# Kernel optimization log

Hardware: AMD Instinct MI355X
Metric: run time of the kernel (lower is better)

Reference implementation:

```python
import jax, jax.numpy as jnp
import numpy as np

BATCH = 10
HID = 128
OUT = 7
MAX_LEN = 2048


def setup_inputs() -> dict:
    key = jax.random.key(0)
    ks = jax.random.split(key, 10)
    h0 = jax.random.normal(ks[0], (1, BATCH, HID), dtype=jnp.float32)
    c0 = jax.random.normal(ks[1], (1, BATCH, HID), dtype=jnp.float32)
    # target is a sequence of one-hot vectors, shape (MAX_LEN+1, 1, OUT)
    tgt_idx = jax.random.randint(ks[2], (MAX_LEN + 1,), 0, OUT)
    target_onehot = jax.nn.one_hot(tgt_idx, OUT, dtype=jnp.float32)[:, None, :]
    # per-step teacher-forcing coin flips (torch.rand(1) < 0.5 externalized)
    tf_mask = jax.random.bernoulli(ks[3], 0.5, (MAX_LEN,))
    # LSTM parameters, torch gate order [i, f, g, o]; k = 1/sqrt(HID) init scale
    k = 1.0 / np.sqrt(HID)
    W_ih = jax.random.uniform(ks[4], (4 * HID, OUT), minval=-k, maxval=k, dtype=jnp.float32)
    W_hh = jax.random.uniform(ks[5], (4 * HID, HID), minval=-k, maxval=k, dtype=jnp.float32)
    b_ih = jax.random.uniform(ks[6], (4 * HID,), minval=-k, maxval=k, dtype=jnp.float32)
    b_hh = jax.random.uniform(ks[7], (4 * HID,), minval=-k, maxval=k, dtype=jnp.float32)
    W_out = jax.random.uniform(ks[8], (OUT, HID), minval=-k, maxval=k, dtype=jnp.float32)
    b_out = jax.random.uniform(ks[9], (OUT,), minval=-k, maxval=k, dtype=jnp.float32)
    return dict(h0=h0, c0=c0, target_onehot=target_onehot, tf_mask=tf_mask,
                W_ih=W_ih, W_hh=W_hh, b_ih=b_ih, b_hh=b_hh, W_out=W_out, b_out=b_out)


def reference(h0, c0, target_onehot, tf_mask, W_ih, W_hh, b_ih, b_hh, W_out, b_out):
    # initial decoder input: one-hot at last class for all 10 batch items
    x0 = jnp.zeros((BATCH, OUT), jnp.float32).at[:, OUT - 1].set(1.0)
    tgt_next = target_onehot[1:MAX_LEN + 1, 0, :]  # (MAX_LEN, OUT), fed at step i
    bias = b_ih + b_hh

    def step(carry, inp):
        h, c, x = carry            # h,c: (B,HID); x: (B,OUT)
        tf, tgt = inp              # tf: scalar bool; tgt: (OUT,)
        xr = jax.nn.relu(x)
        gates = xr @ W_ih.T + h @ W_hh.T + bias          # (B, 4*HID)
        i_g, f_g, g_g, o_g = jnp.split(gates, 4, axis=-1)
        c2 = jax.nn.sigmoid(f_g) * c + jax.nn.sigmoid(i_g) * jnp.tanh(g_g)
        h2 = jax.nn.sigmoid(o_g) * jnp.tanh(c2)
        logits = h2 @ W_out.T + b_out                    # (B, OUT)
        greedy = jax.nn.one_hot(jnp.argmax(logits, axis=-1), OUT, dtype=jnp.float32)
        nxt = jnp.where(tf, jnp.broadcast_to(tgt, (BATCH, OUT)), greedy)
        return (h2, c2, nxt), logits

    (hT, cT, _), logits = jax.lax.scan(
        step, (h0[0], c0[0], x0), (tf_mask, tgt_next))
    logits = jnp.transpose(logits, (1, 0, 2))            # (B, MAX_LEN, OUT)
    log_probs = jax.nn.log_softmax(logits, axis=-1)
    return log_probs, (hT[None], cT[None])
```

## Files before the change

kernel.cpp:

```cpp
#include <hip/hip_runtime.h>
#include <math.h>

#define BATCH 10
#define HID 128
#define OUT 7
#define MAXLEN 2048
#define NG 512
#define NT 512
#define RINGD 512
#define OFF_STATE ((size_t)BATCH * MAXLEN * OUT)

typedef float float2v __attribute__((ext_vector_type(2)));
typedef float float4v __attribute__((ext_vector_type(4)));

__device__ __forceinline__ float sigm_(float x) { return 1.0f / (1.0f + __expf(-x)); }
__device__ __forceinline__ float tanh_(float x) { return 1.0f - 2.0f / (1.0f + __expf(2.0f * x)); }

__device__ __forceinline__ float grp8_sum(float v) {
    v += __int_as_float(__builtin_amdgcn_update_dpp(0, __float_as_int(v), 0xB1, 0xF, 0xF, true));
    v += __int_as_float(__builtin_amdgcn_update_dpp(0, __float_as_int(v), 0x4E, 0xF, 0xF, true));
    v += __int_as_float(__builtin_amdgcn_update_dpp(0, __float_as_int(v), 0x141, 0xF, 0xF, true));
    return v;
}

__global__
__attribute__((amdgpu_flat_work_group_size(NT, NT), amdgpu_waves_per_eu(2, 2)))
void decoder_rnn_kernel(const float* __restrict__ h0,
                        const float* __restrict__ c0,
                        const float* __restrict__ tonehot,
                        const void*  __restrict__ tf_raw,
                        const float* __restrict__ Wih,
                        const float* __restrict__ Whh,
                        const float* __restrict__ bih,
                        const float* __restrict__ bhh,
                        const float* __restrict__ Wout,
                        const float* __restrict__ bout,
                        float* __restrict__ out)
{
    __shared__ __align__(16) float h_lds[HID];
    __shared__ __align__(16) float gates_lds[NG];
    __shared__ float wih_eff[OUT * NG];
    __shared__ float ring[RINGD][OUT];
    __shared__ unsigned char tgt8[MAXLEN];
    __shared__ unsigned char tf8[MAXLEN];
    __shared__ int tf_byte_mode;

    const int t    = threadIdx.x;
    const int lane = t & 63;
    const int wv   = t >> 6;
    const int ksl  = lane & 7;
    const int grp  = lane >> 3;
    const int b    = blockIdx.x;
    const int gbase = wv * 64 + grp * 8;

    float2v wgt2[8][8];
    #pragma unroll
    for (int g = 0; g < 8; g++)
        #pragma unroll
        for (int p = 0; p < 8; p++) {
            const int kk = (p >> 1) * 32 + ksl * 4 + (p & 1) * 2;
            wgt2[g][p] = *(const float2v*)&Whh[(size_t)(gbase + g) * HID + kk];
        }

    float2v lw2[8];
    #pragma unroll
    for (int p = 0; p < 8; p++) { float2v z = {0.f, 0.f}; lw2[p] = z; }
    if (wv < 2 && grp < OUT) {
        #pragma unroll
        for (int p = 0; p < 8; p++) {
            const int kk = (p >> 1) * 32 + ksl * 4 + (p & 1) * 2;
            lw2[p] = *(const float2v*)&Wout[(size_t)grp * HID + kk];
        }
    }

    float boutr[OUT];
    #pragma unroll
    for (int j = 0; j < OUT; j++) boutr[j] = bout[j];

    for (int idx = t; idx < OUT * NG; idx += NT) {
        int x = idx >> 9, g = idx & (NG - 1);
        wih_eff[idx] = Wih[g * OUT + x] + bih[g] + bhh[g];
    }
    if (t == 0) tf_byte_mode = 0;
    for (int s = t; s < MAXLEN; s += NT) {
        const float* row = tonehot + (size_t)(s + 1) * OUT;
        int idx = 0;
        #pragma unroll
        for (int j = 0; j < OUT; j++) if (row[j] > 0.5f) idx = j;
        tgt8[s] = (unsigned char)idx;
    }
    __syncthreads();
    {
        const unsigned char* tb = (const unsigned char*)tf_raw;
        int mis = 0;
        for (int p = t; p < MAXLEN; p += NT)
            if ((p & 3) && tb[p]) mis = 1;
        if (mis) atomicOr(&tf_byte_mode, 1);
    }
    float c_reg = 0.f, hv = 0.f;
    if (t < HID) {
        hv    = h0[b * HID + t];
        c_reg = c0[b * HID + t];
        h_lds[t] = hv;
    }
    __syncthreads();
    if (tf_byte_mode) {
        const unsigned char* tb = (const unsigned char*)tf_raw;
        for (int s = t; s < MAXLEN; s += NT) tf8[s] = (tb[s] != 0);
    } else {
        const int* ti = (const int*)tf_raw;
        for (int s = t; s < MAXLEN; s += NT) tf8[s] = (ti[s] != 0);
    }
    __syncthreads();

    float* outlp = out + (size_t)b * MAXLEN * OUT;

    for (int s = 0; s < MAXLEN; s++) {
        float4v hc[4];
        #pragma unroll
        for (int c = 0; c < 4; c++)
            hc[c] = *(const float4v*)&h_lds[c * 32 + ksl * 4];

        float2v acc[8];
        #pragma unroll
        for (int g = 0; g < 8; g++) { float2v z = {0.f, 0.f}; acc[g] = z; }
        #pragma unroll
        for (int p = 0; p < 8; p++) {
            const float2v hp = (p & 1)
                ? __builtin_shufflevector(hc[p >> 1], hc[p >> 1], 2, 3)
                : __builtin_shufflevector(hc[p >> 1], hc[p >> 1], 0, 1);
            #pragma unroll
            for (int g = 0; g < 8; g++)
                acc[g] = __builtin_elementwise_fma(wgt2[g][p], hp, acc[g]);
        }
        float a[8];
        #pragma unroll
        for (int g = 0; g < 8; g++) a[g] = grp8_sum(acc[g][0] + acc[g][1]);

        int xsel = OUT - 1;
        if (wv < 2) {
            float2v accl = {0.f, 0.f};
            #pragma unroll
            for (int p = 0; p < 8; p++) {
                const float2v hp = (p & 1)
                    ? __builtin_shufflevector(hc[p >> 1], hc[p >> 1], 2, 3)
                    : __builtin_shufflevector(hc[p >> 1], hc[p >> 1], 0, 1);
                accl = __builtin_elementwise_fma(lw2[p], hp, accl);
            }
            const float al = grp8_sum(accl[0] + accl[1]);
            if (s > 0) {
                float lg[OUT];
                lg[0] = __int_as_float(__builtin_amdgcn_readlane(__float_as_int(al),  0)) + boutr[0];
                lg[1] = __int_as_float(__builtin_amdgcn_readlane(__float_as_int(al),  8)) + boutr[1];
                lg[2] = __int_as_float(__builtin_amdgcn_readlane(__float_as_int(al), 16)) + boutr[2];
                lg[3] = __int_as_float(__builtin_amdgcn_readlane(__float_as_int(al), 24)) + boutr[3];
                lg[4] = __int_as_float(__builtin_amdgcn_readlane(__float_as_int(al), 32)) + boutr[4];
                lg[5] = __int_as_float(__builtin_amdgcn_readlane(__float_as_int(al), 40)) + boutr[5];
                lg[6] = __int_as_float(__builtin_amdgcn_readlane(__float_as_int(al), 48)) + boutr[6];
                float bv = lg[0]; int bi = 0;
                #pragma unroll
                for (int j = 1; j < OUT; j++) if (lg[j] > bv) { bv = lg[j]; bi = j; }
                xsel = tf8[s - 1] ? (int)tgt8[s - 1] : bi;
                if (wv == 0 && ksl == 0 && grp < OUT)
                    ring[(s - 1) & (RINGD - 1)][grp] = al;
            }
        }
        if (ksl == 0) {
            float4v g4a, g4b;
            g4a[0] = a[0]; g4a[1] = a[1]; g4a[2] = a[2]; g4a[3] = a[3];
            g4b[0] = a[4]; g4b[1] = a[5]; g4b[2] = a[6]; g4b[3] = a[7];
            *(float4v*)&gates_lds[gbase]     = g4a;
            *(float4v*)&gates_lds[gbase + 4] = g4b;
        }
        __syncthreads();

        if (t < HID) {
            const int xo = xsel * NG;
            float ri = gates_lds[t]           + wih_eff[xo + t];
            float rf = gates_lds[HID + t]     + wih_eff[xo + HID + t];
            float rg = gates_lds[2 * HID + t] + wih_eff[xo + 2 * HID + t];
            float ro = gates_lds[3 * HID + t] + wih_eff[xo + 3 * HID + t];
            float cn = sigm_(rf) * c_reg + sigm_(ri) * tanh_(rg);
            c_reg = cn;
            hv = sigm_(ro) * tanh_(cn);
            h_lds[t] = hv;
        } else if (t >= 256 && (s & 255) == 1 && s > 256) {
            const int step = (s - 257) + (t - 256);
            const int slot = step & (RINGD - 1);
            float v[OUT];
            #pragma unroll
            for (int j = 0; j < OUT; j++) v[j] = ring[slot][j] + boutr[j];
            float mx = v[0];
            #pragma unroll
            for (int j = 1; j < OUT; j++) mx = fmaxf(mx, v[j]);
            float sum = 0.f;
            #pragma unroll
            for (int j = 0; j < OUT; j++) sum += __expf(v[j] - mx);
            const float lse = mx + __logf(sum);
            float* dst = outlp + (size_t)step * OUT;
            #pragma unroll
            for (int j = 0; j < OUT; j++) dst[j] = v[j] - lse;
        }
        __syncthreads();
    }

    if (wv < 2) {
        float2v accl = {0.f, 0.f};
        #pragma unroll
        for (int p = 0; p < 8; p++) {
            const int kk = (p >> 1) * 32 + ksl * 4 + (p & 1) * 2;
            const float2v hp = *(const float2v*)&h_lds[kk];
            accl = __builtin_elementwise_fma(lw2[p], hp, accl);
        }
        const float al = grp8_sum(accl[0] + accl[1]);
        if (wv == 0 && ksl == 0 && grp < OUT)
            ring[(MAXLEN - 1) & (RINGD - 1)][grp] = al;
    }
    __syncthreads();
    if (t < 256) {
        const int step = (MAXLEN - 256) + t;
        const int slot = step & (RINGD - 1);
        float v[OUT];
        #pragma unroll
        for (int j = 0; j < OUT; j++) v[j] = ring[slot][j] + boutr[j];
        float mx = v[0];
        #pragma unroll
        for (int j = 1; j < OUT; j++) mx = fmaxf(mx, v[j]);
        float sum = 0.f;
        #pragma unroll
        for (int j = 0; j < OUT; j++) sum += __expf(v[j] - mx);
        const float lse = mx + __logf(sum);
        float* dst = outlp + (size_t)step * OUT;
        #pragma unroll
        for (int j = 0; j < OUT; j++) dst[j] = v[j] - lse;
    }
    if (t < HID) {
        out[OFF_STATE + b * HID + t] = hv;
        out[OFF_STATE + BATCH * HID + b * HID + t] = c_reg;
    }
}

extern "C" void kernel_launch(void* const* d_in, const int* in_sizes, int n_in,
                              void* d_out, int out_size, void* d_ws, size_t ws_size,
                              hipStream_t stream) {
    const float* h0    = (const float*)d_in[0];
    const float* c0    = (const float*)d_in[1];
    const float* toh   = (const float*)d_in[2];
    const void*  tfm   = (const void*) d_in[3];
    const float* Wih   = (const float*)d_in[4];
    const float* Whh   = (const float*)d_in[5];
    const float* bih   = (const float*)d_in[6];
    const float* bhh   = (const float*)d_in[7];
    const float* Wout  = (const float*)d_in[8];
    const float* bout  = (const float*)d_in[9];
    float* out = (float*)d_out;

    decoder_rnn_kernel<<<dim3(BATCH), dim3(NT), 0, stream>>>(
        h0, c0, toh, tfm, Wih, Whh, bih, bhh, Wout, bout, out);
}
```

Measured before the change: 1.955 ms.

## Remap threads so each 4-lane group owns all four gates of one hidden unit

Threads are reassigned so each group of 4 lanes computes the i, f, g and o gate dot products for one hidden unit, with the input-weight contributions held in registers. This removes the gates LDS round trip and one of the two barriers per step. Double-buffering h lets each step end with a single barrier. Every wave now also computes the output projection and the redundant LSTM cell math, which adds work per step in exchange for shortening the serial critical path.

```diff
diff --git a/kernel.cpp b/kernel.cpp
--- a/kernel.cpp
+++ b/kernel.cpp
@@ -5,7 +5,6 @@
 #define HID 128
 #define OUT 7
 #define MAXLEN 2048
-#define NG 512
 #define NT 512
 #define RINGD 512
 #define OFF_STATE ((size_t)BATCH * MAXLEN * OUT)
@@ -16,10 +15,12 @@
 __device__ __forceinline__ float sigm_(float x) { return 1.0f / (1.0f + __expf(-x)); }
 __device__ __forceinline__ float tanh_(float x) { return 1.0f - 2.0f / (1.0f + __expf(2.0f * x)); }
 
-__device__ __forceinline__ float grp8_sum(float v) {
+__device__ __forceinline__ float2v vlo(float4v v) { return __builtin_shufflevector(v, v, 0, 1); }
+__device__ __forceinline__ float2v vhi(float4v v) { return __builtin_shufflevector(v, v, 2, 3); }
+
+__device__ __forceinline__ float grp4_sum(float v) {
     v += __int_as_float(__builtin_amdgcn_update_dpp(0, __float_as_int(v), 0xB1, 0xF, 0xF, true));
     v += __int_as_float(__builtin_amdgcn_update_dpp(0, __float_as_int(v), 0x4E, 0xF, 0xF, true));
-    v += __int_as_float(__builtin_amdgcn_update_dpp(0, __float_as_int(v), 0x141, 0xF, 0xF, true));
     return v;
 }
 
@@ -37,9 +38,7 @@
                         const float* __restrict__ bout,
                         float* __restrict__ out)
 {
-    __shared__ __align__(16) float h_lds[HID];
-    __shared__ __align__(16) float gates_lds[NG];
-    __shared__ float wih_eff[OUT * NG];
+    __shared__ __align__(16) float h_lds[2][HID];
     __shared__ float ring[RINGD][OUT];
     __shared__ unsigned char tgt8[MAXLEN];
     __shared__ unsigned char tf8[MAXLEN];
@@ -48,45 +47,55 @@
     const int t    = threadIdx.x;
     const int lane = t & 63;
     const int wv   = t >> 6;
-    const int ksl  = lane & 7;
-    const int grp  = lane >> 3;
+    const int ksl  = lane & 3;
+    const int grp  = lane >> 2;
     const int b    = blockIdx.x;
-    const int gbase = wv * 64 + grp * 8;
-
-    float2v wgt2[8][8];
-    #pragma unroll
-    for (int g = 0; g < 8; g++)
-        #pragma unroll
-        for (int p = 0; p < 8; p++) {
-            const int kk = (p >> 1) * 32 + ksl * 4 + (p & 1) * 2;
-            wgt2[g][p] = *(const float2v*)&Whh[(size_t)(gbase + g) * HID + kk];
-        }
-
-    float2v lw2[8];
-    #pragma unroll
-    for (int p = 0; p < 8; p++) { float2v z = {0.f, 0.f}; lw2[p] = z; }
-    if (wv < 2 && grp < OUT) {
-        #pragma unroll
-        for (int p = 0; p < 8; p++) {
-            const int kk = (p >> 1) * 32 + ksl * 4 + (p & 1) * 2;
-            lw2[p] = *(const float2v*)&Wout[(size_t)grp * HID + kk];
-        }
-    }
+    const int j    = wv * 16 + grp;
+
+    float4v wgt[4][8];
+    #pragma unroll
+    for (int q = 0; q < 4; q++)
+        #pragma unroll
+        for (int m = 0; m < 8; m++) {
+            const int kb = ksl * 32 + (((m + 2 * ksl) & 7) << 2);
+            wgt[q][m] = *(const float4v*)&Whh[(size_t)(q * HID + j) * HID + kb];
+        }
+    #pragma unroll
+    for (int q = 0; q < 4; q++)
+        #pragma unroll
+        for (int m = 0; m < 8; m++)
+            asm volatile("" : "+v"(wgt[q][m]));
+
+    float4v lwv[8];
+    #pragma unroll
+    for (int m = 0; m < 8; m++) { float4v z = {0.f, 0.f, 0.f, 0.f}; lwv[m] = z; }
+    if (grp < OUT) {
+        #pragma unroll
+        for (int m = 0; m < 8; m++) {
+            const int kb = ksl * 32 + (((m + 2 * ksl) & 7) << 2);
+            lwv[m] = *(const float4v*)&Wout[(size_t)grp * HID + kb];
+        }
+    }
+
+    float wihr[OUT][4];
+    #pragma unroll
+    for (int x = 0; x < OUT; x++)
+        #pragma unroll
+        for (int q = 0; q < 4; q++) {
+            const int g = q * HID + j;
+            wihr[x][q] = Wih[(size_t)g * OUT + x] + bih[g] + bhh[g];
+        }
 
     float boutr[OUT];
     #pragma unroll
-    for (int j = 0; j < OUT; j++) boutr[j] = bout[j];
-
-    for (int idx = t; idx < OUT * NG; idx += NT) {
-        int x = idx >> 9, g = idx & (NG - 1);
-        wih_eff[idx] = Wih[g * OUT + x] + bih[g] + bhh[g];
-    }
+    for (int jj = 0; jj < OUT; jj++) boutr[jj] = bout[jj];
+
     if (t == 0) tf_byte_mode = 0;
     for (int s = t; s < MAXLEN; s += NT) {
         const float* row = tonehot + (size_t)(s + 1) * OUT;
         int idx = 0;
         #pragma unroll
-        for (int j = 0; j < OUT; j++) if (row[j] > 0.5f) idx = j;
+        for (int jj = 0; jj < OUT; jj++) if (row[jj] > 0.5f) idx = jj;
         tgt8[s] = (unsigned char)idx;
     }
     __syncthreads();
@@ -97,12 +106,9 @@
             if ((p & 3) && tb[p]) mis = 1;
         if (mis) atomicOr(&tf_byte_mode, 1);
     }
-    float c_reg = 0.f, hv = 0.f;
-    if (t < HID) {
-        hv    = h0[b * HID + t];
-        c_reg = c0[b * HID + t];
-        h_lds[t] = hv;
-    }
+    float c_reg = c0[b * HID + j];
+    float hv    = h0[b * HID + j];
+    if (t < HID) h_lds[0][t] = h0[b * HID + t];
     __syncthreads();
     if (tf_byte_mode) {
         const unsigned char* tb = (const unsigned char*)tf_raw;
@@ -116,103 +122,100 @@
     float* outlp = out + (size_t)b * MAXLEN * OUT;
 
     for (int s = 0; s < MAXLEN; s++) {
-        float4v hc[4];
-        #pragma unroll
-        for (int c = 0; c < 4; c++)
-            hc[c] = *(const float4v*)&h_lds[c * 32 + ksl * 4];
-
-        float2v acc[8];
-        #pragma unroll
-        for (int g = 0; g < 8; g++) { float2v z = {0.f, 0.f}; acc[g] = z; }
-        #pragma unroll
-        for (int p = 0; p < 8; p++) {
-            const float2v hp = (p & 1)
-                ? __builtin_shufflevector(hc[p >> 1], hc[p >> 1], 2, 3)
-                : __builtin_shufflevector(hc[p >> 1], hc[p >> 1], 0, 1);
-            #pragma unroll
-            for (int g = 0; g < 8; g++)
-                acc[g] = __builtin_elementwise_fma(wgt2[g][p], hp, acc[g]);
-        }
-        float a[8];
-        #pragma unroll
-        for (int g = 0; g < 8; g++) a[g] = grp8_sum(acc[g][0] + acc[g][1]);
+        const float* hb = h_lds[s & 1];
+        float*       hw = h_lds[(s & 1) ^ 1];
+
+        int tfp = 0, tgp = 0;
+        if (s > 0) { tfp = tf8[s - 1]; tgp = tgt8[s - 1]; }
+
+        float2v acc0 = {0.f,0.f}, acc1 = {0.f,0.f}, acc2 = {0.f,0.f},
+                acc3 = {0.f,0.f}, accl = {0.f,0.f};
+        #pragma unroll
+        for (int m = 0; m < 8; m++) {
+            const int kb = ksl * 32 + (((m + 2 * ksl) & 7) << 2);
+            const float4v h4  = *(const float4v*)&hb[kb];
+            const float2v hlo = vlo(h4), hhi = vhi(h4);
+            acc0 = __builtin_elementwise_fma(vlo(wgt[0][m]), hlo, acc0);
+            acc0 = __builtin_elementwise_fma(vhi(wgt[0][m]), hhi, acc0);
+            acc1 = __builtin_elementwise_fma(vlo(wgt[1][m]), hlo, acc1);
+            acc1 = __builtin_elementwise_fma(vhi(wgt[1][m]), hhi, acc1);
+            acc2 = __builtin_elementwise_fma(vlo(wgt[2][m]), hlo, acc2);
+            acc2 = __builtin_elementwise_fma(vhi(wgt[2][m]), hhi, acc2);
+            acc3 = __builtin_elementwise_fma(vlo(wgt[3][m]), hlo, acc3);
+            acc3 = __builtin_elementwise_fma(vhi(wgt[3][m]), hhi, acc3);
+            accl = __builtin_elementwise_fma(vlo(lwv[m]),    hlo, accl);
+            accl = __builtin_elementwise_fma(vhi(lwv[m]),    hhi, accl);
+        }
+        const float a0 = grp4_sum(acc0[0] + acc0[1]);
+        const float a1 = grp4_sum(acc1[0] + acc1[1]);
+        const float a2 = grp4_sum(acc2[0] + acc2[1]);
+        const float a3 = grp4_sum(acc3[0] + acc3[1]);
+        const float al = grp4_sum(accl[0] + accl[1]);
 
         int xsel = OUT - 1;
-        if (wv < 2) {
-            float2v accl = {0.f, 0.f};
-            #pragma unroll
-            for (int p = 0; p < 8; p++) {
-                const float2v hp = (p & 1)
-                    ? __builtin_shufflevector(hc[p >> 1], hc[p >> 1], 2, 3)
-                    : __builtin_shufflevector(hc[p >> 1], hc[p >> 1], 0, 1);
-                accl = __builtin_elementwise_fma(lw2[p], hp, accl);
-            }
-            const float al = grp8_sum(accl[0] + accl[1]);
-            if (s > 0) {
+        if (s > 0) {
+            if (wv == 0 && ksl == 0 && grp < OUT)
+                ring[(s - 1) & (RINGD - 1)][grp] = al;
+            if (tfp) {
+                xsel = tgp;
+            } else {
                 float lg[OUT];
-                lg[0] = __int_as_float(__builtin_amdgcn_readlane(__float_as_int(al),  0)) + boutr[0];
-                lg[1] = __int_as_float(__builtin_amdgcn_readlane(__float_as_int(al),  8)) + boutr[1];
-                lg[2] = __int_as_float(__builtin_amdgcn_readlane(__float_as_int(al), 16)) + boutr[2];
-                lg[3] = __int_as_float(__builtin_amdgcn_readlane(__float_as_int(al), 24)) + boutr[3];
-                lg[4] = __int_as_float(__builtin_amdgcn_readlane(__float_as_int(al), 32)) + boutr[4];
-                lg[5] = __int_as_float(__builtin_amdgcn_readlane(__float_as_int(al), 40)) + boutr[5];
-                lg[6] = __int_as_float(__builtin_amdgcn_readlane(__float_as_int(al), 48)) + boutr[6];
+                #pragma unroll
+                for (int jj = 0; jj < OUT; jj++)
+                    lg[jj] = __int_as_float(__builtin_amdgcn_readlane(__float_as_int(al), 4 * jj)) + boutr[jj];
                 float bv = lg[0]; int bi = 0;
                 #pragma unroll
-                for (int j = 1; j < OUT; j++) if (lg[j] > bv) { bv = lg[j]; bi = j; }
-                xsel = tf8[s - 1] ? (int)tgt8[s - 1] : bi;
-                if (wv == 0 && ksl == 0 && grp < OUT)
-                    ring[(s - 1) & (RINGD - 1)][grp] = al;
+                for (int jj = 1; jj < OUT; jj++) if (lg[jj] > bv) { bv = lg[jj]; bi = jj; }
+                xsel = bi;
             }
         }
-        if (ksl == 0) {
-            float4v g4a, g4b;
-            g4a[0] = a[0]; g4a[1] = a[1]; g4a[2] = a[2]; g4a[3] = a[3];
-            g4b[0] = a[4]; g4b[1] = a[5]; g4b[2] = a[6]; g4b[3] = a[7];
-            *(float4v*)&gates_lds[gbase]     = g4a;
-            *(float4v*)&gates_lds[gbase + 4] = g4b;
-        }
-        __syncthreads();
-
-        if (t < HID) {
-            const int xo = xsel * NG;
-            float ri = gates_lds[t]           + wih_eff[xo + t];
-            float rf = gates_lds[HID + t]     + wih_eff[xo + HID + t];
-            float rg = gates_lds[2 * HID + t] + wih_eff[xo + 2 * HID + t];
-            float ro = gates_lds[3 * HID + t] + wih_eff[xo + 3 * HID + t];
-            float cn = sigm_(rf) * c_reg + sigm_(ri) * tanh_(rg);
-            c_reg = cn;
-            hv = sigm_(ro) * tanh_(cn);
-            h_lds[t] = hv;
-        } else if (t >= 256 && (s & 255) == 1 && s > 256) {
-            const int step = (s - 257) + (t - 256);
+
+        float w0 = wihr[0][0], w1 = wihr[0][1], w2 = wihr[0][2], w3 = wihr[0][3];
+        #pragma unroll
+        for (int x = 1; x < OUT; x++) {
+            const bool px = (xsel == x);
+            w0 = px ? wihr[x][0] : w0;
+            w1 = px ? wihr[x][1] : w1;
+            w2 = px ? wihr[x][2] : w2;
+            w3 = px ? wihr[x][3] : w3;
+        }
+
+        const float ri = a0 + w0, rf = a1 + w1, rg = a2 + w2, ro = a3 + w3;
+        const float cn = sigm_(rf) * c_reg + sigm_(ri) * tanh_(rg);
+        c_reg = cn;
+        hv = sigm_(ro) * tanh_(cn);
+        if (ksl == 0) hw[j] = hv;
+
+        if (t < 256 && (s & 255) == 1 && s > 256) {
+            const int step = (s - 257) + t;
             const int slot = step & (RINGD - 1);
             float v[OUT];
             #pragma unroll
-            for (int j = 0; j < OUT; j++) v[j] = ring[slot][j] + boutr[j];
+            for (int jj = 0; jj < OUT; jj++) v[jj] = ring[slot][jj] + boutr[jj];
             float mx = v[0];
             #pragma unroll
-            for (int j = 1; j < OUT; j++) mx = fmaxf(mx, v[j]);
+            for (int jj = 1; jj < OUT; jj++) mx = fmaxf(mx, v[jj]);
             float sum = 0.f;
             #pragma unroll
-            for (int j = 0; j < OUT; j++) sum += __expf(v[j] - mx);
+            for (int jj = 0; jj < OUT; jj++) sum += __expf(v[jj] - mx);
             const float lse = mx + __logf(sum);
             float* dst = outlp + (size_t)step * OUT;
             #pragma unroll
-            for (int j = 0; j < OUT; j++) dst[j] = v[j] - lse;
+            for (int jj = 0; jj < OUT; jj++) dst[jj] = v[jj] - lse;
         }
         __syncthreads();
     }
 
-    if (wv < 2) {
+    {
         float2v accl = {0.f, 0.f};
         #pragma unroll
-        for (int p = 0; p < 8; p++) {
-            const int kk = (p >> 1) * 32 + ksl * 4 + (p & 1) * 2;
-            const float2v hp = *(const float2v*)&h_lds[kk];
-            accl = __builtin_elementwise_fma(lw2[p], hp, accl);
-        }
-        const float al = grp8_sum(accl[0] + accl[1]);
+        for (int m = 0; m < 8; m++) {
+            const int kb = ksl * 32 + (((m + 2 * ksl) & 7) << 2);
+            const float4v h4 = *(const float4v*)&h_lds[0][kb];
+            accl = __builtin_elementwise_fma(vlo(lwv[m]), vlo(h4), accl);
+            accl = __builtin_elementwise_fma(vhi(lwv[m]), vhi(h4), accl);
+        }
+        const float al = grp4_sum(accl[0] + accl[1]);
         if (wv == 0 && ksl == 0 && grp < OUT)
             ring[(MAXLEN - 1) & (RINGD - 1)][grp] = al;
     }
@@ -222,21 +225,21 @@
         const int slot = step & (RINGD - 1);
         float v[OUT];
         #pragma unroll
-        for (int j = 0; j < OUT; j++) v[j] = ring[slot][j] + boutr[j];
+        for (int jj = 0; jj < OUT; jj++) v[jj] = ring[slot][jj] + boutr[jj];
         float mx = v[0];
         #pragma unroll
-        for (int j = 1; j < OUT; j++) mx = fmaxf(mx, v[j]);
+        for (int jj = 1; jj < OUT; jj++) mx = fmaxf(mx, v[jj]);
         float sum = 0.f;
         #pragma unroll
-        for (int j = 0; j < OUT; j++) sum += __expf(v[j] - mx);
+        for (int jj = 0; jj < OUT; jj++) sum += __expf(v[jj] - mx);
         const float lse = mx + __logf(sum);
         float* dst = outlp + (size_t)step * OUT;
         #pragma unroll
-        for (int j = 0; j < OUT; j++) dst[j] = v[j] - lse;
-    }
-    if (t < HID) {
-        out[OFF_STATE + b * HID + t] = hv;
-        out[OFF_STATE + BATCH * HID + b * HID + t] = c_reg;
+        for (int jj = 0; jj < OUT; jj++) dst[jj] = v[jj] - lse;
+    }
+    if (ksl == 0) {
+        out[OFF_STATE + b * HID + j] = hv;
+        out[OFF_STATE + BATCH * HID + b * HID + j] = c_reg;
     }
 }
 
```

Result: slower. 2.643 ms (+35.2%).

## Split hidden-state reduction across 16 waves with partial-sum LDS staging

Applied to the files above, without the earlier changes.

Doubles the workgroup to 1024 threads and splits the K dimension of the recurrent matvec across wave pairs, so each thread holds fewer weights and does fewer FMAs per step. The per-wave partial sums are written to four LDS slices and combined by the gate threads. The output projection moves to an LDS copy of Wout split across two waves, and argmax/teacher-forcing selection moves into the gate threads. This shortens the per-step serial critical path, at the cost of more LDS traffic, more waves taking part in each barrier, and an extra reduction stage.

```diff
diff --git a/kernel.cpp b/kernel.cpp
--- a/kernel.cpp
+++ b/kernel.cpp
@@ -5,8 +5,7 @@
 #define HID 128
 #define OUT 7
 #define MAXLEN 2048
-#define NG 512
-#define NT 512
+#define NT 1024
 #define RINGD 512
 #define OFF_STATE ((size_t)BATCH * MAXLEN * OUT)
 
@@ -16,6 +15,18 @@
 __device__ __forceinline__ float sigm_(float x) { return 1.0f / (1.0f + __expf(-x)); }
 __device__ __forceinline__ float tanh_(float x) { return 1.0f - 2.0f / (1.0f + __expf(2.0f * x)); }
 
+__device__ __forceinline__ float2v vlo(float4v v) { return __builtin_shufflevector(v, v, 0, 1); }
+__device__ __forceinline__ float2v vhi(float4v v) { return __builtin_shufflevector(v, v, 2, 3); }
+
+__device__ __forceinline__ void pk_fma(float2v& acc, float2v w, float2v h) {
+    asm("v_pk_fma_f32 %0, %1, %2, %0" : "+v"(acc) : "v"(w), "v"(h));
+}
+
+__device__ __forceinline__ float quad_sum(float v) {
+    v += __int_as_float(__builtin_amdgcn_update_dpp(0, __float_as_int(v), 0xB1, 0xF, 0xF, true));
+    v += __int_as_float(__builtin_amdgcn_update_dpp(0, __float_as_int(v), 0x4E, 0xF, 0xF, true));
+    return v;
+}
 __device__ __forceinline__ float grp8_sum(float v) {
     v += __int_as_float(__builtin_amdgcn_update_dpp(0, __float_as_int(v), 0xB1, 0xF, 0xF, true));
     v += __int_as_float(__builtin_amdgcn_update_dpp(0, __float_as_int(v), 0x4E, 0xF, 0xF, true));
@@ -24,7 +35,7 @@
 }
 
 __global__
-__attribute__((amdgpu_flat_work_group_size(NT, NT), amdgpu_waves_per_eu(2, 2)))
+__attribute__((amdgpu_flat_work_group_size(NT, NT), amdgpu_waves_per_eu(4, 4)))
 void decoder_rnn_kernel(const float* __restrict__ h0,
                         const float* __restrict__ c0,
                         const float* __restrict__ tonehot,
@@ -38,49 +49,44 @@
                         float* __restrict__ out)
 {
     __shared__ __align__(16) float h_lds[HID];
-    __shared__ __align__(16) float gates_lds[NG];
-    __shared__ float wih_eff[OUT * NG];
+    __shared__ __align__(16) float gpart[4][520];
+    __shared__ float wih_eff[OUT * 512];
+    __shared__ float WoutL[8][132];
+    __shared__ float lp[2][8];
     __shared__ float ring[RINGD][OUT];
     __shared__ unsigned char tgt8[MAXLEN];
     __shared__ unsigned char tf8[MAXLEN];
     __shared__ int tf_byte_mode;
 
-    const int t    = threadIdx.x;
-    const int lane = t & 63;
-    const int wv   = t >> 6;
-    const int ksl  = lane & 7;
-    const int grp  = lane >> 3;
-    const int b    = blockIdx.x;
-    const int gbase = wv * 64 + grp * 8;
-
-    float2v wgt2[8][8];
+    const int t     = threadIdx.x;
+    const int lane  = t & 63;
+    const int wv    = t >> 6;
+    const int ksl   = lane & 7;
+    const int grp   = lane >> 3;
+    const int b     = blockIdx.x;
+    const int kset  = wv & 1;
+    const int gw    = wv >> 1;
+    const int gbase = gw * 64 + grp * 8;
+    const int kb    = kset * 64 + ksl * 8;
+
+    float4v wq[8][2];
     #pragma unroll
     for (int g = 0; g < 8; g++)
         #pragma unroll
-        for (int p = 0; p < 8; p++) {
-            const int kk = (p >> 1) * 32 + ksl * 4 + (p & 1) * 2;
-            wgt2[g][p] = *(const float2v*)&Whh[(size_t)(gbase + g) * HID + kk];
-        }
-
-    float2v lw2[8];
-    #pragma unroll
-    for (int p = 0; p < 8; p++) { float2v z = {0.f, 0.f}; lw2[p] = z; }
-    if (wv < 2 && grp < OUT) {
-        #pragma unroll
-        for (int p = 0; p < 8; p++) {
-            const int kk = (p >> 1) * 32 + ksl * 4 + (p & 1) * 2;
-            lw2[p] = *(const float2v*)&Wout[(size_t)grp * HID + kk];
-        }
-    }
+        for (int p = 0; p < 2; p++)
+            wq[g][p] = *(const float4v*)&Whh[(size_t)(gbase + g) * HID + kb + p * 4];
 
     float boutr[OUT];
     #pragma unroll
     for (int j = 0; j < OUT; j++) boutr[j] = bout[j];
 
-    for (int idx = t; idx < OUT * NG; idx += NT) {
-        int x = idx >> 9, g = idx & (NG - 1);
+    for (int idx = t; idx < OUT * 512; idx += NT) {
+        int x = idx >> 9, g = idx & 511;
         wih_eff[idx] = Wih[g * OUT + x] + bih[g] + bhh[g];
     }
+    if (t < HID) WoutL[7][t] = 0.f;
+    for (int idx = t; idx < OUT * HID; idx += NT)
+        WoutL[idx >> 7][idx & 127] = Wout[idx];
     if (t == 0) tf_byte_mode = 0;
     for (int s = t; s < MAXLEN; s += NT) {
         const float* row = tonehot + (size_t)(s + 1) * OUT;
@@ -116,76 +122,78 @@
     float* outlp = out + (size_t)b * MAXLEN * OUT;
 
     for (int s = 0; s < MAXLEN; s++) {
-        float4v hc[4];
-        #pragma unroll
-        for (int c = 0; c < 4; c++)
-            hc[c] = *(const float4v*)&h_lds[c * 32 + ksl * 4];
+        const float4v h0q = *(const float4v*)&h_lds[kb];
+        const float4v h1q = *(const float4v*)&h_lds[kb + 4];
+        const float2v hl0 = vlo(h0q), hh0 = vhi(h0q);
+        const float2v hl1 = vlo(h1q), hh1 = vhi(h1q);
 
         float2v acc[8];
         #pragma unroll
         for (int g = 0; g < 8; g++) { float2v z = {0.f, 0.f}; acc[g] = z; }
         #pragma unroll
-        for (int p = 0; p < 8; p++) {
-            const float2v hp = (p & 1)
-                ? __builtin_shufflevector(hc[p >> 1], hc[p >> 1], 2, 3)
-                : __builtin_shufflevector(hc[p >> 1], hc[p >> 1], 0, 1);
-            #pragma unroll
-            for (int g = 0; g < 8; g++)
-                acc[g] = __builtin_elementwise_fma(wgt2[g][p], hp, acc[g]);
+        for (int g = 0; g < 8; g++) {
+            pk_fma(acc[g], vlo(wq[g][0]), hl0);
+            pk_fma(acc[g], vhi(wq[g][0]), hh0);
+            pk_fma(acc[g], vlo(wq[g][1]), hl1);
+            pk_fma(acc[g], vhi(wq[g][1]), hh1);
         }
         float a[8];
         #pragma unroll
-        for (int g = 0; g < 8; g++) a[g] = grp8_sum(acc[g][0] + acc[g][1]);
-
-        int xsel = OUT - 1;
-        if (wv < 2) {
-            float2v accl = {0.f, 0.f};
-            #pragma unroll
-            for (int p = 0; p < 8; p++) {
-                const float2v hp = (p & 1)
-                    ? __builtin_shufflevector(hc[p >> 1], hc[p >> 1], 2, 3)
-                    : __builtin_shufflevector(hc[p >> 1], hc[p >> 1], 0, 1);
-                accl = __builtin_elementwise_fma(lw2[p], hp, accl);
-            }
-            const float al = grp8_sum(accl[0] + accl[1]);
-            if (s > 0) {
-                float lg[OUT];
-                lg[0] = __int_as_float(__builtin_amdgcn_readlane(__float_as_int(al),  0)) + boutr[0];
-                lg[1] = __int_as_float(__builtin_amdgcn_readlane(__float_as_int(al),  8)) + boutr[1];
-                lg[2] = __int_as_float(__builtin_amdgcn_readlane(__float_as_int(al), 16)) + boutr[2];
-                lg[3] = __int_as_float(__builtin_amdgcn_readlane(__float_as_int(al), 24)) + boutr[3];
-                lg[4] = __int_as_float(__builtin_amdgcn_readlane(__float_as_int(al), 32)) + boutr[4];
-                lg[5] = __int_as_float(__builtin_amdgcn_readlane(__float_as_int(al), 40)) + boutr[5];
-                lg[6] = __int_as_float(__builtin_amdgcn_readlane(__float_as_int(al), 48)) + boutr[6];
-                float bv = lg[0]; int bi = 0;
-                #pragma unroll
-                for (int j = 1; j < OUT; j++) if (lg[j] > bv) { bv = lg[j]; bi = j; }
-                xsel = tf8[s - 1] ? (int)tgt8[s - 1] : bi;
-                if (wv == 0 && ksl == 0 && grp < OUT)
-                    ring[(s - 1) & (RINGD - 1)][grp] = al;
-            }
-        }
-        if (ksl == 0) {
+        for (int g = 0; g < 8; g++) a[g] = quad_sum(acc[g][0] + acc[g][1]);
+        if ((ksl & 3) == 0) {
+            const int pl = (kset << 1) | (ksl >> 2);
             float4v g4a, g4b;
             g4a[0] = a[0]; g4a[1] = a[1]; g4a[2] = a[2]; g4a[3] = a[3];
             g4b[0] = a[4]; g4b[1] = a[5]; g4b[2] = a[6]; g4b[3] = a[7];
-            *(float4v*)&gates_lds[gbase]     = g4a;
-            *(float4v*)&gates_lds[gbase + 4] = g4b;
+            *(float4v*)&gpart[pl][gbase]     = g4a;
+            *(float4v*)&gpart[pl][gbase + 4] = g4b;
+        }
+        if (wv < 2) {
+            const float4v wo0 = *(const float4v*)&WoutL[grp][kb];
+            const float4v wo1 = *(const float4v*)&WoutL[grp][kb + 4];
+            float2v la = {0.f, 0.f};
+            pk_fma(la, vlo(wo0), hl0);
+            pk_fma(la, vhi(wo0), hh0);
+            pk_fma(la, vlo(wo1), hl1);
+            pk_fma(la, vhi(wo1), hh1);
+            const float al = grp8_sum(la[0] + la[1]);
+            if (ksl == 0 && grp < OUT) lp[wv][grp] = al;
         }
         __syncthreads();
 
         if (t < HID) {
-            const int xo = xsel * NG;
-            float ri = gates_lds[t]           + wih_eff[xo + t];
-            float rf = gates_lds[HID + t]     + wih_eff[xo + HID + t];
-            float rg = gates_lds[2 * HID + t] + wih_eff[xo + 2 * HID + t];
-            float ro = gates_lds[3 * HID + t] + wih_eff[xo + 3 * HID + t];
-            float cn = sigm_(rf) * c_reg + sigm_(ri) * tanh_(rg);
+            const float ps0 = (gpart[0][t] + gpart[1][t]) + (gpart[2][t] + gpart[3][t]);
+            const float ps1 = (gpart[0][128 + t] + gpart[1][128 + t]) + (gpart[2][128 + t] + gpart[3][128 + t]);
+            const float ps2 = (gpart[0][256 + t] + gpart[1][256 + t]) + (gpart[2][256 + t] + gpart[3][256 + t]);
+            const float ps3 = (gpart[0][384 + t] + gpart[1][384 + t]) + (gpart[2][384 + t] + gpart[3][384 + t]);
+            int xsel = OUT - 1;
+            if (s > 0) {
+                const int tfp = tf8[s - 1];
+                if (t < OUT) ring[(s - 1) & (RINGD - 1)][t] = lp[0][t] + lp[1][t];
+                if (tfp) {
+                    xsel = tgt8[s - 1];
+                } else {
+                    float lg[OUT];
+                    #pragma unroll
+                    for (int j = 0; j < OUT; j++)
+                        lg[j] = lp[0][j] + lp[1][j] + boutr[j];
+                    float bv = lg[0]; int bi = 0;
+                    #pragma unroll
+                    for (int j = 1; j < OUT; j++) if (lg[j] > bv) { bv = lg[j]; bi = j; }
+                    xsel = bi;
+                }
+            }
+            const int xo = xsel * 512;
+            const float ri = ps0 + wih_eff[xo + t];
+            const float rf = ps1 + wih_eff[xo + 128 + t];
+            const float rg = ps2 + wih_eff[xo + 256 + t];
+            const float ro = ps3 + wih_eff[xo + 384 + t];
+            const float cn = sigm_(rf) * c_reg + sigm_(ri) * tanh_(rg);
             c_reg = cn;
             hv = sigm_(ro) * tanh_(cn);
             h_lds[t] = hv;
-        } else if (t >= 256 && (s & 255) == 1 && s > 256) {
-            const int step = (s - 257) + (t - 256);
+        } else if (t >= 128 && t < 384 && (s & 255) == 1 && s > 256) {
+            const int step = (s - 257) + (t - 128);
             const int slot = step & (RINGD - 1);
             float v[OUT];
             #pragma unroll
@@ -205,17 +213,21 @@
     }
 
     if (wv < 2) {
-        float2v accl = {0.f, 0.f};
-        #pragma unroll
-        for (int p = 0; p < 8; p++) {
-            const int kk = (p >> 1) * 32 + ksl * 4 + (p & 1) * 2;
-            const float2v hp = *(const float2v*)&h_lds[kk];
-            accl = __builtin_elementwise_fma(lw2[p], hp, accl);
-        }
-        const float al = grp8_sum(accl[0] + accl[1]);
-        if (wv == 0 && ksl == 0 && grp < OUT)
-            ring[(MAXLEN - 1) & (RINGD - 1)][grp] = al;
-    }
+        const float4v h0q = *(const float4v*)&h_lds[kb];
+        const float4v h1q = *(const float4v*)&h_lds[kb + 4];
+        const float4v wo0 = *(const float4v*)&WoutL[grp][kb];
+        const float4v wo1 = *(const float4v*)&WoutL[grp][kb + 4];
+        float2v la = {0.f, 0.f};
+        pk_fma(la, vlo(wo0), vlo(h0q));
+        pk_fma(la, vhi(wo0), vhi(h0q));
+        pk_fma(la, vlo(wo1), vlo(h1q));
+        pk_fma(la, vhi(wo1), vhi(h1q));
+        const float al = grp8_sum(la[0] + la[1]);
+        if (ksl == 0 && grp < OUT) lp[wv][grp] = al;
+    }
+    __syncthreads();
+    if (t < OUT)
+        ring[(MAXLEN - 1) & (RINGD - 1)][t] = lp[0][t] + lp[1][t];
     __syncthreads();
     if (t < 256) {
         const int step = (MAXLEN - 256) + t;
```

Measured after the change: 2.407 ms. 1.23x slower.
